# Kernel optimization log

Hardware: AMD Instinct MI355X
Metric: run time of the kernel (lower is better)

## Reference

```python
import jax, jax.numpy as jnp
import numpy as np

N_NODES = 100000
N_EDGES = 1600000
N_GRAPHS = 512
IN_DIM, HID, GOUT, SCAL = 256, 128, 64, 2


def setup_inputs() -> dict:
    key = jax.random.key(0)
    ks = jax.random.split(key, 12)
    x = jax.random.normal(ks[0], (N_NODES, IN_DIM), dtype=jnp.float32)
    edge_index = jax.random.randint(ks[1], (2, N_EDGES), 0, N_NODES, dtype=jnp.int64)
    batch = jnp.sort(jax.random.randint(ks[2], (N_NODES,), 0, N_GRAPHS, dtype=jnp.int64))
    scalars = jax.random.normal(ks[3], (N_GRAPHS, SCAL), dtype=jnp.float32)
    def lin(k, fan_in, fan_out):
        s = 1.0 / np.sqrt(fan_in)
        kw, kb = jax.random.split(k)
        W = jax.random.uniform(kw, (fan_in, fan_out), minval=-s, maxval=s, dtype=jnp.float32)
        b = jax.random.uniform(kb, (fan_out,), minval=-s, maxval=s, dtype=jnp.float32)
        return W, b
    W1, b1 = lin(ks[4], IN_DIM, HID)
    W2, b2 = lin(ks[5], HID, GOUT)
    W3, b3 = lin(ks[6], GOUT + SCAL, HID)
    W4, b4 = lin(ks[7], HID, 1)
    return {"x": x, "edge_index": edge_index, "batch": batch, "scalars": scalars,
            "W1": W1, "b1": b1, "W2": W2, "b2": b2,
            "W3": W3, "b3": b3, "W4": W4, "b4": b4}


def gcn_conv(x, W, b, src, dst, num_nodes):
    # PyG GCNConv: h = x @ W; add self-loops; norm = d^-1/2[src] * d^-1/2[dst]
    # with deg = in-degree (on dst) + 1 (self-loop); scatter-add into dst.
    h = x @ W  # [N, F]
    deg = jax.ops.segment_sum(jnp.ones((src.shape[0],), h.dtype), dst,
                              num_segments=num_nodes) + 1.0
    dinv = jax.lax.rsqrt(deg)  # [N]
    norm = dinv[src] * dinv[dst]  # [E]
    agg = jax.ops.segment_sum(h[src] * norm[:, None], dst, num_segments=num_nodes)
    agg = agg + h * (dinv * dinv)[:, None]  # self-loop contribution
    return agg + b


def global_mean_pool(x, batch, num_graphs):
    s = jax.ops.segment_sum(x, batch, num_segments=num_graphs)
    cnt = jax.ops.segment_sum(jnp.ones((x.shape[0],), x.dtype), batch,
                              num_segments=num_graphs)
    return s / jnp.maximum(cnt, 1.0)[:, None]


def reference(x, edge_index, batch, scalars, W1, b1, W2, b2, W3, b3, W4, b4):
    src, dst = edge_index[0], edge_index[1]
    h = jax.nn.relu(gcn_conv(x, W1, b1, src, dst, N_NODES))
    h = gcn_conv(h, W2, b2, src, dst, N_NODES)
    emb = global_mean_pool(h, batch, N_GRAPHS)  # [G, GOUT]
    combined = jnp.concatenate([emb, scalars], axis=1)  # [G, GOUT+SCAL]
    out = jax.nn.sigmoid(jax.nn.relu(combined @ W3 + b3) @ W4 + b4)
    return out.reshape(-1, 1)
```

## Files before the change

### kernel.cpp

```cpp
#include <hip/hip_runtime.h>

#define NN 100000
#define NE 1600000
#define NG 512
#define NPARTS 500
#define PW 200
#define NCHUNKS 128
#define CE 12500
#define NCNT (NPARTS * NCHUNKS)

typedef unsigned int uint;
typedef unsigned short ushort;
typedef __bf16 bf16x8 __attribute__((ext_vector_type(8)));
typedef float f32x4 __attribute__((ext_vector_type(4)));

__device__ inline uint f2bf2(float a, float b) {
  uint ua = __float_as_uint(a), ub = __float_as_uint(b);
  ua += 0x7fff + ((ua >> 16) & 1);
  ub += 0x7fff + ((ub >> 16) & 1);
  return (ua >> 16) | (ub & 0xffff0000u);
}
__device__ inline ushort f2bf(float f) {
  uint u = __float_as_uint(f);
  u += 0x7fff + ((u >> 16) & 1);
  return (ushort)(u >> 16);
}
__device__ inline float2 bf2f(uint v) {
  float2 r;
  r.x = __uint_as_float(v << 16);
  r.y = __uint_as_float(v & 0xffff0000u);
  return r;
}
__device__ inline uint relu2(uint u) {
  uint lo = (u & 0x8000u) ? 0u : (u & 0xFFFFu);
  uint hi = (u & 0x80000000u) ? 0u : (u & 0xFFFF0000u);
  return lo | hi;
}

__global__ __launch_bounds__(256) void prep(const float* __restrict__ W1, uint* __restrict__ w1t,
                                            const float* __restrict__ W2, uint* __restrict__ w2t,
                                            const int* __restrict__ dst, int* __restrict__ cnt) {
  int b = blockIdx.x, t = threadIdx.x;
  if (b < 192) {
    __shared__ float col[256];
    const float* W; uint* Wt; int K, N, n;
    if (b < 128) { W = W1; Wt = w1t; K = 256; N = 128; n = b; }
    else         { W = W2; Wt = w2t; K = 128; N = 64;  n = b - 128; }
    if (t < K) col[t] = W[(size_t)t * N + n];
    __syncthreads();
    if (t < K / 2) Wt[(size_t)n * (K / 2) + t] = f2bf2(col[2 * t], col[2 * t + 1]);
  } else {
    __shared__ int h[NPARTS];
    int c = b - 192;
    for (int i = t; i < NPARTS; i += 256) h[i] = 0;
    __syncthreads();
    int beg = c * CE;
    for (int j = t; j < CE; j += 256) atomicAdd(&h[dst[beg + j] / PW], 1);
    __syncthreads();
    for (int i = t; i < NPARTS; i += 256) cnt[i * NCHUNKS + c] = h[i];
  }
}

__global__ void scan1(const int* __restrict__ in, int* __restrict__ out,
                      int* __restrict__ bsum, int n) {
  __shared__ int s[256];
  int t = threadIdx.x;
  int i = blockIdx.x * 256 + t;
  int v = (i < n) ? in[i] : 0;
  s[t] = v;
  __syncthreads();
  for (int off = 1; off < 256; off <<= 1) {
    int add = (t >= off) ? s[t - off] : 0;
    __syncthreads();
    s[t] += add;
    __syncthreads();
  }
  if (i < n) out[i] = s[t] - v;
  if (t == 255) bsum[blockIdx.x] = s[255];
}

__global__ void scan2(int* __restrict__ bsum, int nb) {
  __shared__ int s[512];
  int t = threadIdx.x;
  int v = (t < nb) ? bsum[t] : 0;
  s[t] = v;
  __syncthreads();
  for (int off = 1; off < 512; off <<= 1) {
    int add = (t >= off) ? s[t - off] : 0;
    __syncthreads();
    s[t] += add;
    __syncthreads();
  }
  if (t < nb) bsum[t] = s[t] - v;
}

__global__ __launch_bounds__(256) void bucket_scatter(const int* __restrict__ src,
                                                      const int* __restrict__ dst,
                                                      const int* __restrict__ off,
                                                      const int* __restrict__ bsum,
                                                      uint* __restrict__ pk) {
  __shared__ int cur[NPARTS];
  int t = threadIdx.x, c = blockIdx.x;
  for (int i = t; i < NPARTS; i += 256) {
    int idx = i * NCHUNKS + c;
    cur[i] = off[idx] + bsum[idx >> 8];
  }
  __syncthreads();
  int beg = c * CE;
  for (int j = t; j < CE; j += 256) {
    int d = dst[beg + j];
    int p = d / PW;
    int pos = atomicAdd(&cur[p], 1);
    pk[pos] = (uint)src[beg + j] | ((uint)(d - p * PW) << 17);
  }
}

__global__ __launch_bounds__(256) void csr_finalize(const uint* __restrict__ pk,
                                                    const int* __restrict__ off,
                                                    const int* __restrict__ bsum,
                                                    int* __restrict__ row_off,
                                                    float* __restrict__ dinv,
                                                    int* __restrict__ csr) {
  __shared__ int hist[PW];
  __shared__ int cur[PW];
  __shared__ int s[256];
  int p = blockIdx.x, t = threadIdx.x;
  int idx0 = p * NCHUNKS;
  int base = off[idx0] + bsum[idx0 >> 8];
  int endp = NE;
  if (p < NPARTS - 1) {
    int idx1 = (p + 1) * NCHUNKS;
    endp = off[idx1] + bsum[idx1 >> 8];
  }
  if (t < PW) hist[t] = 0;
  __syncthreads();
  for (int j = base + t; j < endp; j += 256) atomicAdd(&hist[pk[j] >> 17], 1);
  __syncthreads();
  int v = (t < PW) ? hist[t] : 0;
  s[t] = v;
  __syncthreads();
  for (int o = 1; o < 256; o <<= 1) {
    int add = (t >= o) ? s[t - o] : 0;
    __syncthreads();
    s[t] += add;
    __syncthreads();
  }
  if (t < PW) {
    int excl = base + (s[t] - v);
    int node = p * PW + t;
    row_off[node] = excl;
    dinv[node]    = rsqrtf((float)v + 1.0f);
    cur[t] = excl;
  }
  if (p == NPARTS - 1 && t == 0) row_off[NN] = NE;
  __syncthreads();
  for (int j = base + t; j < endp; j += 256) {
    uint e = pk[j];
    int pos = atomicAdd(&cur[e >> 17], 1);
    csr[pos] = (int)(e & 0x1FFFFu);
  }
}

template<int K, int N, int WM, int WN, int A_BF16, int RELU>
__global__ __launch_bounds__(256) void gemm_direct(const void* __restrict__ Av,
                                                   const uint* __restrict__ Bt,
                                                   const float* __restrict__ dinv,
                                                   ushort* __restrict__ Cb, int M) {
  constexpr int NW = N / WN;
  constexpr int NT = NW / 16;
  __shared__ __align__(16) char bsm[N * K * 2];
  const int tid  = threadIdx.x;
  const int wid  = tid >> 6;
  const int lane = tid & 63;
  const int wm   = wid % WM;
  const int wn   = wid / WM;
  const int l15  = lane & 15;
  const int lk   = lane >> 4;
  const int blockRow = blockIdx.x * (WM * 32);

  constexpr int UPR = K / 8;
  constexpr int TOT = N * K / 8;
#pragma unroll
  for (int i0 = 0; i0 < TOT; i0 += 256) {
    int i = i0 + tid;
    uint4 v = reinterpret_cast<const uint4*>(Bt)[i];
    int n = i / UPR, c = i % UPR;
    int byte = (n * (K * 2) + c * 16) ^ ((n & 7) << 4);
    *reinterpret_cast<uint4*>(bsm + byte) = v;
  }
  __syncthreads();

  f32x4 acc[2][NT];
#pragma unroll
  for (int i = 0; i < 2; ++i)
#pragma unroll
    for (int j = 0; j < NT; ++j) acc[i][j] = (f32x4){0.f, 0.f, 0.f, 0.f};

#pragma unroll
  for (int kk = 0; kk < K / 32; ++kk) {
    bf16x8 af[2], bfr[NT];
#pragma unroll
    for (int mt = 0; mt < 2; ++mt) {
      int grow = blockRow + wm * 32 + mt * 16 + l15;
      int row = grow < M ? grow : M - 1;
      if (A_BF16) {
        uint4 va = *reinterpret_cast<const uint4*>((const uint*)Av + (size_t)row * (K / 2) + kk * 16 + lk * 4);
        if (RELU) { va.x = relu2(va.x); va.y = relu2(va.y); va.z = relu2(va.z); va.w = relu2(va.w); }
        af[mt] = __builtin_bit_cast(bf16x8, va);
      } else {
        const float4* p = reinterpret_cast<const float4*>((const float*)Av + (size_t)row * K + kk * 32 + lk * 8);
        float4 f0 = p[0], f1 = p[1];
        uint4 va;
        va.x = f2bf2(f0.x, f0.y); va.y = f2bf2(f0.z, f0.w);
        va.z = f2bf2(f1.x, f1.y); va.w = f2bf2(f1.z, f1.w);
        af[mt] = __builtin_bit_cast(bf16x8, va);
      }
    }
#pragma unroll
    for (int nt = 0; nt < NT; ++nt) {
      int n = wn * NW + nt * 16 + l15;
      int byte = (n * (K * 2) + kk * 64 + lk * 16) ^ ((n & 7) << 4);
      bfr[nt] = __builtin_bit_cast(bf16x8, *reinterpret_cast<uint4*>(bsm + byte));
    }
#pragma unroll
    for (int mt = 0; mt < 2; ++mt)
#pragma unroll
      for (int nt = 0; nt < NT; ++nt)
        acc[mt][nt] = __builtin_amdgcn_mfma_f32_16x16x32_bf16(af[mt], bfr[nt], acc[mt][nt], 0, 0, 0);
  }

#pragma unroll
  for (int mt = 0; mt < 2; ++mt) {
    int rbase = blockRow + wm * 32 + mt * 16 + lk * 4;
#pragma unroll
    for (int j = 0; j < 4; ++j) {
      int grow = rbase + j;
      if (grow < M) {
        float d = dinv[grow];
#pragma unroll
        for (int nt = 0; nt < NT; ++nt) {
          int gcol = wn * NW + nt * 16 + l15;
          Cb[(size_t)grow * N + gcol] = f2bf(acc[mt][nt][j] * d);
        }
      }
    }
  }
}

__global__ __launch_bounds__(256) void agg_csr_f128_v2(const uint4* __restrict__ hs,
                                                       const float* __restrict__ dinv,
                                                       const float* __restrict__ bias,
                                                       const int* __restrict__ row_off,
                                                       const int* __restrict__ csr,
                                                       uint4* __restrict__ outb, int N) {
  int node = blockIdx.x * 4 + (threadIdx.x >> 6);
  if (node >= N) return;
  int lane = threadIdx.x & 63;
  int sl = lane >> 4;
  int c4 = lane & 15;
  int beg = row_off[node], end = row_off[node + 1];
  float a0=0,a1=0,a2=0,a3=0,a4=0,a5=0,a6=0,a7=0;
  int j = beg;
  for (; j + 16 <= end; j += 16) {
    int s0 = csr[j + sl];
    int s1 = csr[j + 4 + sl];
    int s2 = csr[j + 8 + sl];
    int s3 = csr[j + 12 + sl];
    uint4 v0 = hs[(size_t)s0 * 16 + c4];
    uint4 v1 = hs[(size_t)s1 * 16 + c4];
    uint4 v2 = hs[(size_t)s2 * 16 + c4];
    uint4 v3 = hs[(size_t)s3 * 16 + c4];
    float2 f;
    f = bf2f(v0.x); a0+=f.x; a1+=f.y;  f = bf2f(v0.y); a2+=f.x; a3+=f.y;
    f = bf2f(v0.z); a4+=f.x; a5+=f.y;  f = bf2f(v0.w); a6+=f.x; a7+=f.y;
    f = bf2f(v1.x); a0+=f.x; a1+=f.y;  f = bf2f(v1.y); a2+=f.x; a3+=f.y;
    f = bf2f(v1.z); a4+=f.x; a5+=f.y;  f = bf2f(v1.w); a6+=f.x; a7+=f.y;
    f = bf2f(v2.x); a0+=f.x; a1+=f.y;  f = bf2f(v2.y); a2+=f.x; a3+=f.y;
    f = bf2f(v2.z); a4+=f.x; a5+=f.y;  f = bf2f(v2.w); a6+=f.x; a7+=f.y;
    f = bf2f(v3.x); a0+=f.x; a1+=f.y;  f = bf2f(v3.y); a2+=f.x; a3+=f.y;
    f = bf2f(v3.z); a4+=f.x; a5+=f.y;  f = bf2f(v3.w); a6+=f.x; a7+=f.y;
  }
  for (; j + 4 <= end; j += 4) {
    int s0 = csr[j + sl];
    uint4 v0 = hs[(size_t)s0 * 16 + c4];
    float2 f;
    f = bf2f(v0.x); a0+=f.x; a1+=f.y;  f = bf2f(v0.y); a2+=f.x; a3+=f.y;
    f = bf2f(v0.z); a4+=f.x; a5+=f.y;  f = bf2f(v0.w); a6+=f.x; a7+=f.y;
  }
  if (j + sl < end) {
    int s0 = csr[j + sl];
    uint4 v0 = hs[(size_t)s0 * 16 + c4];
    float2 f;
    f = bf2f(v0.x); a0+=f.x; a1+=f.y;  f = bf2f(v0.y); a2+=f.x; a3+=f.y;
    f = bf2f(v0.z); a4+=f.x; a5+=f.y;  f = bf2f(v0.w); a6+=f.x; a7+=f.y;
  }
  a0 += __shfl_xor(a0, 16); a1 += __shfl_xor(a1, 16); a2 += __shfl_xor(a2, 16); a3 += __shfl_xor(a3, 16);
  a4 += __shfl_xor(a4, 16); a5 += __shfl_xor(a5, 16); a6 += __shfl_xor(a6, 16); a7 += __shfl_xor(a7, 16);
  a0 += __shfl_xor(a0, 32); a1 += __shfl_xor(a1, 32); a2 += __shfl_xor(a2, 32); a3 += __shfl_xor(a3, 32);
  a4 += __shfl_xor(a4, 32); a5 += __shfl_xor(a5, 32); a6 += __shfl_xor(a6, 32); a7 += __shfl_xor(a7, 32);
  if (sl == 0) {
    uint4 v = hs[(size_t)node * 16 + c4];
    float2 f;
    f = bf2f(v.x); a0+=f.x; a1+=f.y;  f = bf2f(v.y); a2+=f.x; a3+=f.y;
    f = bf2f(v.z); a4+=f.x; a5+=f.y;  f = bf2f(v.w); a6+=f.x; a7+=f.y;
    float d = dinv[node];
    const float4* bp = reinterpret_cast<const float4*>(bias);
    float4 b0 = bp[c4 * 2], b1 = bp[c4 * 2 + 1];
    uint4 o;
    o.x = f2bf2(fmaf(a0, d, b0.x), fmaf(a1, d, b0.y));
    o.y = f2bf2(fmaf(a2, d, b0.z), fmaf(a3, d, b0.w));
    o.z = f2bf2(fmaf(a4, d, b1.x), fmaf(a5, d, b1.y));
    o.w = f2bf2(fmaf(a6, d, b1.z), fmaf(a7, d, b1.w));
    outb[(size_t)node * 16 + c4] = o;
  }
}

__global__ __launch_bounds__(256) void agg_csr_f64_v2(const uint4* __restrict__ hs,
                                                      const float* __restrict__ dinv,
                                                      const int* __restrict__ row_off,
                                                      const int* __restrict__ csr,
                                                      float* __restrict__ out, int N) {
  int node = blockIdx.x * 4 + (threadIdx.x >> 6);
  if (node >= N) return;
  int lane = threadIdx.x & 63;
  int sl = lane >> 3;
  int c4 = lane & 7;
  int beg = row_off[node], end = row_off[node + 1];
  float a0=0,a1=0,a2=0,a3=0,a4=0,a5=0,a6=0,a7=0;
  int j = beg;
  for (; j + 16 <= end; j += 16) {
    int s0 = csr[j + sl];
    int s1 = csr[j + 8 + sl];
    uint4 v0 = hs[(size_t)s0 * 8 + c4];
    uint4 v1 = hs[(size_t)s1 * 8 + c4];
    float2 f;
    f = bf2f(v0.x); a0+=f.x; a1+=f.y;  f = bf2f(v0.y); a2+=f.x; a3+=f.y;
    f = bf2f(v0.z); a4+=f.x; a5+=f.y;  f = bf2f(v0.w); a6+=f.x; a7+=f.y;
    f = bf2f(v1.x); a0+=f.x; a1+=f.y;  f = bf2f(v1.y); a2+=f.x; a3+=f.y;
    f = bf2f(v1.z); a4+=f.x; a5+=f.y;  f = bf2f(v1.w); a6+=f.x; a7+=f.y;
  }
  for (; j + 8 <= end; j += 8) {
    int s0 = csr[j + sl];
    uint4 v0 = hs[(size_t)s0 * 8 + c4];
    float2 f;
    f = bf2f(v0.x); a0+=f.x; a1+=f.y;  f = bf2f(v0.y); a2+=f.x; a3+=f.y;
    f = bf2f(v0.z); a4+=f.x; a5+=f.y;  f = bf2f(v0.w); a6+=f.x; a7+=f.y;
  }
  if (j + sl < end) {
    int s0 = csr[j + sl];
    uint4 v0 = hs[(size_t)s0 * 8 + c4];
    float2 f;
    f = bf2f(v0.x); a0+=f.x; a1+=f.y;  f = bf2f(v0.y); a2+=f.x; a3+=f.y;
    f = bf2f(v0.z); a4+=f.x; a5+=f.y;  f = bf2f(v0.w); a6+=f.x; a7+=f.y;
  }
  a0 += __shfl_xor(a0, 8);  a1 += __shfl_xor(a1, 8);  a2 += __shfl_xor(a2, 8);  a3 += __shfl_xor(a3, 8);
  a4 += __shfl_xor(a4, 8);  a5 += __shfl_xor(a5, 8);  a6 += __shfl_xor(a6, 8);  a7 += __shfl_xor(a7, 8);
  a0 += __shfl_xor(a0, 16); a1 += __shfl_xor(a1, 16); a2 += __shfl_xor(a2, 16); a3 += __shfl_xor(a3, 16);
  a4 += __shfl_xor(a4, 16); a5 += __shfl_xor(a5, 16); a6 += __shfl_xor(a6, 16); a7 += __shfl_xor(a7, 16);
  a0 += __shfl_xor(a0, 32); a1 += __shfl_xor(a1, 32); a2 += __shfl_xor(a2, 32); a3 += __shfl_xor(a3, 32);
  a4 += __shfl_xor(a4, 32); a5 += __shfl_xor(a5, 32); a6 += __shfl_xor(a6, 32); a7 += __shfl_xor(a7, 32);
  if (sl == 0) {
    uint4 v = hs[(size_t)node * 8 + c4];
    float2 f;
    f = bf2f(v.x); a0+=f.x; a1+=f.y;  f = bf2f(v.y); a2+=f.x; a3+=f.y;
    f = bf2f(v.z); a4+=f.x; a5+=f.y;  f = bf2f(v.w); a6+=f.x; a7+=f.y;
    float d = dinv[node];
    float4 o0 = make_float4(a0 * d, a1 * d, a2 * d, a3 * d);
    float4 o1 = make_float4(a4 * d, a5 * d, a6 * d, a7 * d);
    float4* op = reinterpret_cast<float4*>(out + (size_t)node * 64 + c4 * 8);
    op[0] = o0;
    op[1] = o1;
  }
}

__global__ __launch_bounds__(256) void pool_mlp(const float* __restrict__ h,
                                                const int* __restrict__ batch,
                                                const float* __restrict__ scalars,
                                                const float* __restrict__ b2,
                                                const float* __restrict__ W3,
                                                const float* __restrict__ b3,
                                                const float* __restrict__ W4,
                                                const float* __restrict__ b4,
                                                float* __restrict__ out, int N) {
  int g = blockIdx.x;
  int t = threadIdx.x;
  int col = t & 63, rr = t >> 6;
  __shared__ int range[2];
  __shared__ float part[4][64];
  __shared__ float comb[66];
  __shared__ float red[2];
  if (t < 2) {
    int target = g + t;
    int lo = 0, hi = N;
    while (lo < hi) { int mid = (lo + hi) >> 1; if (batch[mid] < target) lo = mid + 1; else hi = mid; }
    range[t] = lo;
  }
  __syncthreads();
  int beg = range[0], end = range[1];
  float s = 0.f;
  for (int i = beg + rr; i < end; i += 4) s += h[(size_t)i * 64 + col];
  part[rr][col] = s;
  __syncthreads();
  if (rr == 0) {
    float tot = (part[0][col] + part[1][col]) + (part[2][col] + part[3][col]);
    comb[col] = tot / fmaxf((float)(end - beg), 1.f) + b2[col];
  } else if (t == 64 || t == 65) {
    comb[t] = scalars[g * 2 + (t - 64)];
  }
  __syncthreads();
  if (t < 128) {
    float hh = b3[t];
#pragma unroll
    for (int k = 0; k < 66; ++k) hh += comb[k] * W3[k * 128 + t];
    hh = fmaxf(hh, 0.f);
    float p = hh * W4[t];
#pragma unroll
    for (int off = 32; off > 0; off >>= 1) p += __shfl_down(p, off);
    if ((t & 63) == 0) red[t >> 6] = p;
  }
  __syncthreads();
  if (t == 0) {
    float sum = red[0] + red[1] + b4[0];
    out[g] = 1.f / (1.f + expf(-sum));
  }
}

extern "C" void kernel_launch(void* const* d_in, const int* in_sizes, int n_in,
                              void* d_out, int out_size, void* d_ws, size_t ws_size,
                              hipStream_t stream) {
  const float* x       = (const float*)d_in[0];
  const int*   ei      = (const int*)d_in[1];
  const int*   src     = ei;
  const int*   dstp    = ei + NE;
  const int*   batch   = (const int*)d_in[2];
  const float* scalars = (const float*)d_in[3];
  const float* W1 = (const float*)d_in[4];  const float* b1 = (const float*)d_in[5];
  const float* W2 = (const float*)d_in[6];  const float* b2 = (const float*)d_in[7];
  const float* W3 = (const float*)d_in[8];  const float* b3 = (const float*)d_in[9];
  const float* W4 = (const float*)d_in[10]; const float* b4 = (const float*)d_in[11];
  float* out = (float*)d_out;

  uint*  ws      = (uint*)d_ws;
  uint*  w1t     = ws;
  uint*  w2t     = ws + 16384;
  uint*  hsb     = ws + 20480;
  uint*  agg1b   = hsb + 6400000;
  float* dinv    = (float*)(agg1b + 6400000);
  int*   row_off = (int*)(dinv + NN);
  int*   csr     = row_off + NN + 4;
  uint*  pk      = (uint*)(csr + NE);
  int*   cnt     = (int*)(pk + NE);
  int*   bsum    = cnt + NCNT;

  prep<<<320, 256, 0, stream>>>(W1, w1t, W2, w2t, dstp, cnt);

  scan1<<<(NCNT + 255) / 256, 256, 0, stream>>>(cnt, cnt, bsum, NCNT);
  scan2<<<1, 512, 0, stream>>>(bsum, (NCNT + 255) / 256);
  bucket_scatter<<<NCHUNKS, 256, 0, stream>>>(src, dstp, cnt, bsum, pk);
  csr_finalize<<<NPARTS, 256, 0, stream>>>(pk, cnt, bsum, row_off, dinv, csr);

  gemm_direct<256, 128, 4, 1, 0, 0><<<(NN + 127) / 128, 256, 0, stream>>>(
      x, w1t, dinv, (ushort*)hsb, NN);
  agg_csr_f128_v2<<<(NN + 3) / 4, 256, 0, stream>>>((const uint4*)hsb, dinv, b1,
                                                    row_off, csr, (uint4*)agg1b, NN);

  gemm_direct<128, 64, 4, 1, 1, 1><<<(NN + 127) / 128, 256, 0, stream>>>(
      agg1b, w2t, dinv, (ushort*)hsb, NN);
  agg_csr_f64_v2<<<(NN + 3) / 4, 256, 0, stream>>>((const uint4*)hsb, dinv,
                                                   row_off, csr, (float*)agg1b, NN);

  pool_mlp<<<NG, 256, 0, stream>>>((const float*)agg1b, batch, scalars, b2,
                                   W3, b3, W4, b4, out, NN);
}
```

Measured before the change: 233.2 us.

## Slice SpMM aggregation by feature column groups across blocks

Both CSR aggregation kernels are reorganized so each block handles one feature slice (of 8 column groups) for 32 nodes, with 8 nodes per wavefront and a small number of lanes per node splitting the edges. Blocks with the same node chunk but different slices sit next to each other in launch order, so the same gathered rows are meant to be reused through cache, and the working set per slice is smaller. The manual unrolling is dropped in favour of a simple strided loop, and the bounds check is removed on the assumption that the node count divides by 32. The trade-offs are more redundant csr/row_off reads (repeated for every slice) and shorter, less coalesced gather segments.

After: 501.8 us. 2.15x slower.

```diff
diff --git a/kernel.cpp b/kernel.cpp
--- a/kernel.cpp
+++ b/kernel.cpp
@@ -247,57 +247,33 @@
   }
 }
 
-__global__ __launch_bounds__(256) void agg_csr_f128_v2(const uint4* __restrict__ hs,
+__global__ __launch_bounds__(256) void agg_f128_sliced(const uint4* __restrict__ hs,
                                                        const float* __restrict__ dinv,
                                                        const float* __restrict__ bias,
                                                        const int* __restrict__ row_off,
                                                        const int* __restrict__ csr,
-                                                       uint4* __restrict__ outb, int N) {
-  int node = blockIdx.x * 4 + (threadIdx.x >> 6);
-  if (node >= N) return;
-  int lane = threadIdx.x & 63;
-  int sl = lane >> 4;
-  int c4 = lane & 15;
+                                                       uint4* __restrict__ outb) {
+  int grp   = blockIdx.x & 7;
+  int chunk = blockIdx.x >> 3;
+  int wid   = threadIdx.x >> 6;
+  int lane  = threadIdx.x & 63;
+  int node  = chunk * 32 + wid * 8 + (lane >> 3);
+  int sl    = (lane >> 1) & 3;
+  int cc    = lane & 1;
+  int c4    = grp * 2 + cc;
   int beg = row_off[node], end = row_off[node + 1];
   float a0=0,a1=0,a2=0,a3=0,a4=0,a5=0,a6=0,a7=0;
-  int j = beg;
-  for (; j + 16 <= end; j += 16) {
-    int s0 = csr[j + sl];
-    int s1 = csr[j + 4 + sl];
-    int s2 = csr[j + 8 + sl];
-    int s3 = csr[j + 12 + sl];
-    uint4 v0 = hs[(size_t)s0 * 16 + c4];
-    uint4 v1 = hs[(size_t)s1 * 16 + c4];
-    uint4 v2 = hs[(size_t)s2 * 16 + c4];
-    uint4 v3 = hs[(size_t)s3 * 16 + c4];
+  for (int j = beg + sl; j < end; j += 4) {
+    int s = csr[j];
+    uint4 v = hs[(size_t)s * 16 + c4];
     float2 f;
-    f = bf2f(v0.x); a0+=f.x; a1+=f.y;  f = bf2f(v0.y); a2+=f.x; a3+=f.y;
-    f = bf2f(v0.z); a4+=f.x; a5+=f.y;  f = bf2f(v0.w); a6+=f.x; a7+=f.y;
-    f = bf2f(v1.x); a0+=f.x; a1+=f.y;  f = bf2f(v1.y); a2+=f.x; a3+=f.y;
-    f = bf2f(v1.z); a4+=f.x; a5+=f.y;  f = bf2f(v1.w); a6+=f.x; a7+=f.y;
-    f = bf2f(v2.x); a0+=f.x; a1+=f.y;  f = bf2f(v2.y); a2+=f.x; a3+=f.y;
-    f = bf2f(v2.z); a4+=f.x; a5+=f.y;  f = bf2f(v2.w); a6+=f.x; a7+=f.y;
-    f = bf2f(v3.x); a0+=f.x; a1+=f.y;  f = bf2f(v3.y); a2+=f.x; a3+=f.y;
-    f = bf2f(v3.z); a4+=f.x; a5+=f.y;  f = bf2f(v3.w); a6+=f.x; a7+=f.y;
-  }
-  for (; j + 4 <= end; j += 4) {
-    int s0 = csr[j + sl];
-    uint4 v0 = hs[(size_t)s0 * 16 + c4];
-    float2 f;
-    f = bf2f(v0.x); a0+=f.x; a1+=f.y;  f = bf2f(v0.y); a2+=f.x; a3+=f.y;
-    f = bf2f(v0.z); a4+=f.x; a5+=f.y;  f = bf2f(v0.w); a6+=f.x; a7+=f.y;
-  }
-  if (j + sl < end) {
-    int s0 = csr[j + sl];
-    uint4 v0 = hs[(size_t)s0 * 16 + c4];
-    float2 f;
-    f = bf2f(v0.x); a0+=f.x; a1+=f.y;  f = bf2f(v0.y); a2+=f.x; a3+=f.y;
-    f = bf2f(v0.z); a4+=f.x; a5+=f.y;  f = bf2f(v0.w); a6+=f.x; a7+=f.y;
-  }
-  a0 += __shfl_xor(a0, 16); a1 += __shfl_xor(a1, 16); a2 += __shfl_xor(a2, 16); a3 += __shfl_xor(a3, 16);
-  a4 += __shfl_xor(a4, 16); a5 += __shfl_xor(a5, 16); a6 += __shfl_xor(a6, 16); a7 += __shfl_xor(a7, 16);
-  a0 += __shfl_xor(a0, 32); a1 += __shfl_xor(a1, 32); a2 += __shfl_xor(a2, 32); a3 += __shfl_xor(a3, 32);
-  a4 += __shfl_xor(a4, 32); a5 += __shfl_xor(a5, 32); a6 += __shfl_xor(a6, 32); a7 += __shfl_xor(a7, 32);
+    f = bf2f(v.x); a0+=f.x; a1+=f.y;  f = bf2f(v.y); a2+=f.x; a3+=f.y;
+    f = bf2f(v.z); a4+=f.x; a5+=f.y;  f = bf2f(v.w); a6+=f.x; a7+=f.y;
+  }
+  a0 += __shfl_xor(a0, 2); a1 += __shfl_xor(a1, 2); a2 += __shfl_xor(a2, 2); a3 += __shfl_xor(a3, 2);
+  a4 += __shfl_xor(a4, 2); a5 += __shfl_xor(a5, 2); a6 += __shfl_xor(a6, 2); a7 += __shfl_xor(a7, 2);
+  a0 += __shfl_xor(a0, 4); a1 += __shfl_xor(a1, 4); a2 += __shfl_xor(a2, 4); a3 += __shfl_xor(a3, 4);
+  a4 += __shfl_xor(a4, 4); a5 += __shfl_xor(a5, 4); a6 += __shfl_xor(a6, 4); a7 += __shfl_xor(a7, 4);
   if (sl == 0) {
     uint4 v = hs[(size_t)node * 16 + c4];
     float2 f;
@@ -315,61 +291,41 @@
   }
 }
 
-__global__ __launch_bounds__(256) void agg_csr_f64_v2(const uint4* __restrict__ hs,
+__global__ __launch_bounds__(256) void agg_f64_sliced(const uint4* __restrict__ hs,
                                                       const float* __restrict__ dinv,
                                                       const int* __restrict__ row_off,
                                                       const int* __restrict__ csr,
-                                                      float* __restrict__ out, int N) {
-  int node = blockIdx.x * 4 + (threadIdx.x >> 6);
-  if (node >= N) return;
-  int lane = threadIdx.x & 63;
-  int sl = lane >> 3;
-  int c4 = lane & 7;
+                                                      float* __restrict__ out) {
+  int grp   = blockIdx.x & 7;
+  int chunk = blockIdx.x >> 3;
+  int wid   = threadIdx.x >> 6;
+  int lane  = threadIdx.x & 63;
+  int node  = chunk * 32 + wid * 8 + (lane >> 3);
+  int sl    = lane & 7;
   int beg = row_off[node], end = row_off[node + 1];
   float a0=0,a1=0,a2=0,a3=0,a4=0,a5=0,a6=0,a7=0;
-  int j = beg;
-  for (; j + 16 <= end; j += 16) {
-    int s0 = csr[j + sl];
-    int s1 = csr[j + 8 + sl];
-    uint4 v0 = hs[(size_t)s0 * 8 + c4];
-    uint4 v1 = hs[(size_t)s1 * 8 + c4];
+  for (int j = beg + sl; j < end; j += 8) {
+    int s = csr[j];
+    uint4 v = hs[(size_t)s * 8 + grp];
     float2 f;
-    f = bf2f(v0.x); a0+=f.x; a1+=f.y;  f = bf2f(v0.y); a2+=f.x; a3+=f.y;
-    f = bf2f(v0.z); a4+=f.x; a5+=f.y;  f = bf2f(v0.w); a6+=f.x; a7+=f.y;
-    f = bf2f(v1.x); a0+=f.x; a1+=f.y;  f = bf2f(v1.y); a2+=f.x; a3+=f.y;
-    f = bf2f(v1.z); a4+=f.x; a5+=f.y;  f = bf2f(v1.w); a6+=f.x; a7+=f.y;
-  }
-  for (; j + 8 <= end; j += 8) {
-    int s0 = csr[j + sl];
-    uint4 v0 = hs[(size_t)s0 * 8 + c4];
-    float2 f;
-    f = bf2f(v0.x); a0+=f.x; a1+=f.y;  f = bf2f(v0.y); a2+=f.x; a3+=f.y;
-    f = bf2f(v0.z); a4+=f.x; a5+=f.y;  f = bf2f(v0.w); a6+=f.x; a7+=f.y;
-  }
-  if (j + sl < end) {
-    int s0 = csr[j + sl];
-    uint4 v0 = hs[(size_t)s0 * 8 + c4];
-    float2 f;
-    f = bf2f(v0.x); a0+=f.x; a1+=f.y;  f = bf2f(v0.y); a2+=f.x; a3+=f.y;
-    f = bf2f(v0.z); a4+=f.x; a5+=f.y;  f = bf2f(v0.w); a6+=f.x; a7+=f.y;
-  }
-  a0 += __shfl_xor(a0, 8);  a1 += __shfl_xor(a1, 8);  a2 += __shfl_xor(a2, 8);  a3 += __shfl_xor(a3, 8);
-  a4 += __shfl_xor(a4, 8);  a5 += __shfl_xor(a5, 8);  a6 += __shfl_xor(a6, 8);  a7 += __shfl_xor(a7, 8);
-  a0 += __shfl_xor(a0, 16); a1 += __shfl_xor(a1, 16); a2 += __shfl_xor(a2, 16); a3 += __shfl_xor(a3, 16);
-  a4 += __shfl_xor(a4, 16); a5 += __shfl_xor(a5, 16); a6 += __shfl_xor(a6, 16); a7 += __shfl_xor(a7, 16);
-  a0 += __shfl_xor(a0, 32); a1 += __shfl_xor(a1, 32); a2 += __shfl_xor(a2, 32); a3 += __shfl_xor(a3, 32);
-  a4 += __shfl_xor(a4, 32); a5 += __shfl_xor(a5, 32); a6 += __shfl_xor(a6, 32); a7 += __shfl_xor(a7, 32);
+    f = bf2f(v.x); a0+=f.x; a1+=f.y;  f = bf2f(v.y); a2+=f.x; a3+=f.y;
+    f = bf2f(v.z); a4+=f.x; a5+=f.y;  f = bf2f(v.w); a6+=f.x; a7+=f.y;
+  }
+  a0 += __shfl_xor(a0, 1); a1 += __shfl_xor(a1, 1); a2 += __shfl_xor(a2, 1); a3 += __shfl_xor(a3, 1);
+  a4 += __shfl_xor(a4, 1); a5 += __shfl_xor(a5, 1); a6 += __shfl_xor(a6, 1); a7 += __shfl_xor(a7, 1);
+  a0 += __shfl_xor(a0, 2); a1 += __shfl_xor(a1, 2); a2 += __shfl_xor(a2, 2); a3 += __shfl_xor(a3, 2);
+  a4 += __shfl_xor(a4, 2); a5 += __shfl_xor(a5, 2); a6 += __shfl_xor(a6, 2); a7 += __shfl_xor(a7, 2);
+  a0 += __shfl_xor(a0, 4); a1 += __shfl_xor(a1, 4); a2 += __shfl_xor(a2, 4); a3 += __shfl_xor(a3, 4);
+  a4 += __shfl_xor(a4, 4); a5 += __shfl_xor(a5, 4); a6 += __shfl_xor(a6, 4); a7 += __shfl_xor(a7, 4);
   if (sl == 0) {
-    uint4 v = hs[(size_t)node * 8 + c4];
+    uint4 v = hs[(size_t)node * 8 + grp];
     float2 f;
     f = bf2f(v.x); a0+=f.x; a1+=f.y;  f = bf2f(v.y); a2+=f.x; a3+=f.y;
     f = bf2f(v.z); a4+=f.x; a5+=f.y;  f = bf2f(v.w); a6+=f.x; a7+=f.y;
     float d = dinv[node];
-    float4 o0 = make_float4(a0 * d, a1 * d, a2 * d, a3 * d);
-    float4 o1 = make_float4(a4 * d, a5 * d, a6 * d, a7 * d);
-    float4* op = reinterpret_cast<float4*>(out + (size_t)node * 64 + c4 * 8);
-    op[0] = o0;
-    op[1] = o1;
+    float4* op = reinterpret_cast<float4*>(out + (size_t)node * 64 + grp * 8);
+    op[0] = make_float4(a0 * d, a1 * d, a2 * d, a3 * d);
+    op[1] = make_float4(a4 * d, a5 * d, a6 * d, a7 * d);
   }
 }
 
@@ -461,13 +417,13 @@
 
   gemm_direct<256, 128, 4, 1, 0, 0><<<(NN + 127) / 128, 256, 0, stream>>>(
       x, w1t, dinv, (ushort*)hsb, NN);
-  agg_csr_f128_v2<<<(NN + 3) / 4, 256, 0, stream>>>((const uint4*)hsb, dinv, b1,
-                                                    row_off, csr, (uint4*)agg1b, NN);
+  agg_f128_sliced<<<(NN / 32) * 8, 256, 0, stream>>>((const uint4*)hsb, dinv, b1,
+                                                     row_off, csr, (uint4*)agg1b);
 
   gemm_direct<128, 64, 4, 1, 1, 1><<<(NN + 127) / 128, 256, 0, stream>>>(
       agg1b, w2t, dinv, (ushort*)hsb, NN);
-  agg_csr_f64_v2<<<(NN + 3) / 4, 256, 0, stream>>>((const uint4*)hsb, dinv,
-                                                   row_off, csr, (float*)agg1b, NN);
+  agg_f64_sliced<<<(NN / 32) * 8, 256, 0, stream>>>((const uint4*)hsb, dinv,
+                                                    row_off, csr, (float*)agg1b);
 
   pool_mlp<<<NG, 256, 0, stream>>>((const float*)agg1b, batch, scalars, b2,
                                    W3, b3, W4, b4, out, NN);
```
